# Kernel tuning notes

Hardware: AMD Instinct MI355X
Metric: run time of the kernel (lower is better)

## Reference

```python
import jax, jax.numpy as jnp
import numpy as np

INPUT_DIM = 1024
ATTN_DIM = 1024
B, S = 4, 4096


def setup_inputs() -> dict:
    key = jax.random.key(0)
    ks = jax.random.split(key, 9)
    def xavier(k, shape):
        fan_in, fan_out = shape[1], shape[0]
        limit = (6.0 / (fan_in + fan_out)) ** 0.5
        return jax.random.uniform(k, shape, jnp.float32, -limit, limit)
    return {
        "x": jax.random.normal(ks[0], (B, S, INPUT_DIM), jnp.float32),
        "Wq": xavier(ks[1], (ATTN_DIM, INPUT_DIM)),
        "bq": jnp.zeros((ATTN_DIM,), jnp.float32),
        "Wk": xavier(ks[2], (ATTN_DIM, INPUT_DIM)),
        "bk": jnp.zeros((ATTN_DIM,), jnp.float32),
        "Wv": xavier(ks[3], (ATTN_DIM, INPUT_DIM)),
        "bv": jnp.zeros((ATTN_DIM,), jnp.float32),
        "Wo": xavier(ks[4], (INPUT_DIM, ATTN_DIM)),
        "bo": jnp.zeros((INPUT_DIM,), jnp.float32),
    }


def reference(x, Wq, bq, Wk, bk, Wv, bv, Wo, bo):
    # Linear layers: y = x @ W^T + b (torch convention, W is [out, in])
    q = jnp.einsum("bsd,ad->bsa", x, Wq) + bq  # [B,S,A]
    k = jnp.einsum("bsd,ad->bsa", x, Wk) + bk
    v = jnp.einsum("bsd,ad->bsa", x, Wv) + bv
    scale = 1.0 / jnp.sqrt(jnp.float32(q.shape[-1]))
    scores = jnp.einsum("bqa,bka->bqk", q, k) * scale  # [B,S,S] full score matrix
    attn = jax.nn.softmax(scores, axis=-1)
    ctx = jnp.einsum("bqk,bka->bqa", attn, v)  # [B,S,A]
    return jnp.einsum("bsa,da->bsd", ctx, Wo) + bo
```

## Files before the change

kernel.cpp:

```cpp
#include <hip/hip_runtime.h>
#include <hip/hip_bf16.h>
#include <cstdint>

#define GLOBAL_AS __attribute__((address_space(1)))
#define LDS_AS    __attribute__((address_space(3)))

typedef __bf16 v8bf __attribute__((ext_vector_type(8)));
typedef __bf16 v4bf __attribute__((ext_vector_type(4)));
typedef float  v4f  __attribute__((ext_vector_type(4)));

struct P2 { __bf16* p[2]; };
struct P4 { __bf16* p[4]; };

template <int SWZ, int LBN, int LBM, int LNZ>
__device__ __forceinline__ void remap(int& bn, int& bm, int& bz) {
    if constexpr (!SWZ) {
        bn = blockIdx.x; bm = blockIdx.y; bz = blockIdx.z;
    } else {
        const unsigned f = blockIdx.x + (blockIdx.y << LBN) + (blockIdx.z << (LBN + LBM));
        const unsigned xcd = f & 7u, slot = f >> 3;
        constexpr unsigned T = (1u << (LNZ + LBM)) >> 3;
        const unsigned p = xcd * T + (slot >> LBN);
        bn = (int)(slot & ((1u << LBN) - 1u));
        bm = (int)(p & ((1u << LBM) - 1u));
        bz = (int)(p >> LBM);
    }
}

__device__ __forceinline__ void kloop(const __bf16* __restrict__ Abase, int lda,
                                      const __bf16* __restrict__ Bbase, int ldb,
                                      int K, __bf16* As, __bf16* Bs,
                                      v4f (&acc)[4][4], int wave, int lane)
{
    const int wr = wave >> 1, wc = wave & 1;
    const int quad = lane >> 4, l15 = lane & 15;
    const int ar = lane >> 2;
    const int ac = (lane & 3) * 8;

    for (int kt = 0; kt < K; kt += 32) {
        __syncthreads();
#pragma unroll
        for (int i = 0; i < 2; i++) {
            const int r = wave * 32 + i * 16;
            __builtin_amdgcn_global_load_lds(
                (const GLOBAL_AS void*)(Abase + (size_t)(r + ar) * lda + kt + ac),
                (LDS_AS void*)(As + r * 32), 16, 0, 0);
            __builtin_amdgcn_global_load_lds(
                (const GLOBAL_AS void*)(Bbase + (size_t)(r + ar) * ldb + kt + ac),
                (LDS_AS void*)(Bs + r * 32), 16, 0, 0);
        }
        __syncthreads();

        v8bf aF[4], bF[4];
#pragma unroll
        for (int i = 0; i < 4; i++)
            aF[i] = *(const v8bf*)(As + (wr * 64 + i * 16 + l15) * 32 + quad * 8);
#pragma unroll
        for (int j = 0; j < 4; j++)
            bF[j] = *(const v8bf*)(Bs + (wc * 64 + j * 16 + l15) * 32 + quad * 8);
#pragma unroll
        for (int i = 0; i < 4; i++)
#pragma unroll
            for (int j = 0; j < 4; j++)
                acc[i][j] = __builtin_amdgcn_mfma_f32_16x16x32_bf16(aF[i], bF[j], acc[i][j], 0, 0, 0);
    }
}

template <typename OutT, int SWZ, int LBN, int LBM, int LNZ>
__global__ void gemm_bt(const __bf16* __restrict__ A, int lda, long long sA,
                        const __bf16* __restrict__ B, int ldb, long long sB,
                        OutT* __restrict__ C, int ldc, long long sC,
                        int K,
                        const float* __restrict__ bias_col,
                        const float* __restrict__ bias_row)
{
    __shared__ __align__(16) __bf16 As[128 * 32];
    __shared__ __align__(16) __bf16 Bs[128 * 32];
    const int tid = threadIdx.x, wave = tid >> 6, lane = tid & 63;
    const int wr = wave >> 1, wc = wave & 1, quad = lane >> 4, l15 = lane & 15;
    int bn, bm, bz;
    remap<SWZ, LBN, LBM, LNZ>(bn, bm, bz);
    A += (long long)bz * sA;
    B += (long long)bz * sB;
    C += (long long)bz * sC;

    v4f acc[4][4];
#pragma unroll
    for (int i = 0; i < 4; i++)
#pragma unroll
        for (int j = 0; j < 4; j++) acc[i][j] = (v4f){0.f, 0.f, 0.f, 0.f};

    kloop(A + (size_t)(bm * 128) * lda, lda, B + (size_t)(bn * 128) * ldb, ldb,
          K, As, Bs, acc, wave, lane);

#pragma unroll
    for (int i = 0; i < 4; i++) {
        const int row0 = bm * 128 + wr * 64 + i * 16 + quad * 4;
#pragma unroll
        for (int j = 0; j < 4; j++) {
            const int col = bn * 128 + wc * 64 + j * 16 + l15;
            const float bc = bias_col ? bias_col[col] : 0.f;
#pragma unroll
            for (int r = 0; r < 4; r++) {
                float v = acc[i][j][r] + bc;
                if (bias_row) v += bias_row[row0 + r];
                C[(size_t)(row0 + r) * ldc + col] = (OutT)v;
            }
        }
    }
}

template <int SWZ, int LBN, int LBM, int LNZ>
__global__ void gemm_exp(const __bf16* __restrict__ A, int lda, long long sA,
                         const __bf16* __restrict__ B, int ldb, long long sB,
                         P2 Eout, int ldc,
                         float* __restrict__ rowsum, int rsStride, int K)
{
    __shared__ __align__(16) __bf16 As[128 * 32];
    __shared__ __align__(16) __bf16 Bs[128 * 32];
    const int tid = threadIdx.x, wave = tid >> 6, lane = tid & 63;
    const int wr = wave >> 1, wc = wave & 1, quad = lane >> 4, l15 = lane & 15;
    int bn, bm, bz;
    remap<SWZ, LBN, LBM, LNZ>(bn, bm, bz);
    A += (long long)bz * sA;
    B += (long long)bz * sB;
    __bf16* C = Eout.p[bz];
    float* rs = rowsum + (long long)bz * rsStride;

    v4f acc[4][4];
#pragma unroll
    for (int i = 0; i < 4; i++)
#pragma unroll
        for (int j = 0; j < 4; j++) acc[i][j] = (v4f){0.f, 0.f, 0.f, 0.f};

    kloop(A + (size_t)(bm * 128) * lda, lda, B + (size_t)(bn * 128) * ldb, ldb,
          K, As, Bs, acc, wave, lane);

#pragma unroll
    for (int i = 0; i < 4; i++) {
        const int row0 = bm * 128 + wr * 64 + i * 16 + quad * 4;
        float part[4] = {0.f, 0.f, 0.f, 0.f};
#pragma unroll
        for (int j = 0; j < 4; j++) {
            const int col = bn * 128 + wc * 64 + j * 16 + l15;
#pragma unroll
            for (int r = 0; r < 4; r++) {
                float e = __expf(acc[i][j][r]);
                C[(size_t)(row0 + r) * ldc + col] = (__bf16)e;
                part[r] += e;
            }
        }
#pragma unroll
        for (int r = 0; r < 4; r++) {
#pragma unroll
            for (int off = 1; off < 16; off <<= 1)
                part[r] += __shfl_xor(part[r], off, 16);
        }
        if (l15 == 0) {
#pragma unroll
            for (int r = 0; r < 4; r++) atomicAdd(&rs[row0 + r], part[r]);
        }
    }
}

template <int SWZ, int LBN, int LBM, int LNZ>
__global__ void gemm_av(P4 Ain, int lda,
                        const __bf16* __restrict__ Bv, int ldb, long long sB,
                        __bf16* __restrict__ C, int ldc, long long sC,
                        const float* __restrict__ rowsum, int rsStride, int K)
{
    __shared__ __align__(16) __bf16 As[128 * 32];
    __shared__ __align__(16) __bf16 Bs[128 * 32];
    const int tid = threadIdx.x, wave = tid >> 6, lane = tid & 63;
    const int wr = wave >> 1, wc = wave & 1, quad = lane >> 4, l15 = lane & 15;
    int bn, bm, bz;
    remap<SWZ, LBN, LBM, LNZ>(bn, bm, bz);
    const __bf16* A = Ain.p[bz];
    const __bf16* B = Bv + (long long)bz * sB;
    C += (long long)bz * sC;
    const float* rs = rowsum + (long long)bz * rsStride;

    v4f acc[4][4];
#pragma unroll
    for (int i = 0; i < 4; i++)
#pragma unroll
        for (int j = 0; j < 4; j++) acc[i][j] = (v4f){0.f, 0.f, 0.f, 0.f};

    kloop(A + (size_t)(bm * 128) * lda, lda, B + (size_t)(bn * 128) * ldb, ldb,
          K, As, Bs, acc, wave, lane);

#pragma unroll
    for (int i = 0; i < 4; i++) {
        const int row0 = bm * 128 + wr * 64 + i * 16 + quad * 4;
        float inv[4];
#pragma unroll
        for (int r = 0; r < 4; r++) inv[r] = 1.0f / rs[row0 + r];
#pragma unroll
        for (int j = 0; j < 4; j++) {
            const int col = bn * 128 + wc * 64 + j * 16 + l15;
#pragma unroll
            for (int r = 0; r < 4; r++)
                C[(size_t)(row0 + r) * ldc + col] = (__bf16)(acc[i][j][r] * inv[r]);
        }
    }
}

__global__ void cvt_f32_bf16(const float* __restrict__ in, __bf16* __restrict__ out, int n4) {
    int i = blockIdx.x * blockDim.x + threadIdx.x;
    if (i >= n4) return;
    float4 f = ((const float4*)in)[i];
    v4bf o;
    o[0] = (__bf16)f.x; o[1] = (__bf16)f.y; o[2] = (__bf16)f.z; o[3] = (__bf16)f.w;
    ((v4bf*)out)[i] = o;
}

__global__ void cvt_w4(const float* __restrict__ w0, const float* __restrict__ w1,
                       const float* __restrict__ w2, const float* __restrict__ w3,
                       __bf16* __restrict__ dst, int n4, float wscale0) {
    const float* s = blockIdx.y == 0 ? w0 : blockIdx.y == 1 ? w1 : blockIdx.y == 2 ? w2 : w3;
    const float sc = blockIdx.y == 0 ? wscale0 : 1.f;
    int i = blockIdx.x * blockDim.x + threadIdx.x;
    if (i >= n4) return;
    float4 f = ((const float4*)s)[i];
    v4bf o;
    o[0] = (__bf16)(f.x * sc); o[1] = (__bf16)(f.y * sc);
    o[2] = (__bf16)(f.z * sc); o[3] = (__bf16)(f.w * sc);
    ((v4bf*)(dst + (size_t)blockIdx.y * n4 * 4))[i] = o;
}

__global__ void concat_bias2(const float* __restrict__ b0, const float* __restrict__ b1,
                             float* __restrict__ dst, int n, float s0) {
    int i = blockIdx.x * blockDim.x + threadIdx.x;
    if (i < n) dst[i] = b0[i] * s0;
    else if (i < 2 * n) dst[i] = b1[i - n];
}

__global__ void zero_f32(float* __restrict__ p, int n) {
    int i = blockIdx.x * blockDim.x + threadIdx.x;
    if (i < n) p[i] = 0.f;
}

extern "C" void kernel_launch(void* const* d_in, const int* in_sizes, int n_in,
                              void* d_out, int out_size, void* d_ws, size_t ws_size,
                              hipStream_t stream)
{
    const float* x  = (const float*)d_in[0];
    const float* Wq = (const float*)d_in[1];
    const float* bq = (const float*)d_in[2];
    const float* Wk = (const float*)d_in[3];
    const float* bk = (const float*)d_in[4];
    const float* Wv = (const float*)d_in[5];
    const float* bv = (const float*)d_in[6];
    const float* Wo = (const float*)d_in[7];
    const float* bo = (const float*)d_in[8];
    float* out = (float*)d_out;

    constexpr int B = 4, S = 4096, D = 1024;
    constexpr long long MS = (long long)B * S;
    constexpr float scale = 0.03125f;

    char* w = (char*)d_ws;
    size_t used = 0;
    auto alloc = [&](size_t bytes) -> char* {
        char* p = w + used;
        used += (bytes + 255) & ~(size_t)255;
        return p;
    };
    __bf16* xb  = (__bf16*)alloc((size_t)MS * D * 2);
    __bf16* wqb = (__bf16*)alloc(4 * (size_t)D * D * 2);
    __bf16* wvb = wqb + 2 * (size_t)D * D;
    __bf16* wob = wqb + 3 * (size_t)D * D;
    float*  bqk = (float*)alloc(2 * D * 4);
    float*  rsm = (float*)alloc((size_t)B * S * 4);
    __bf16* qk  = (__bf16*)alloc((size_t)MS * 2 * D * 2);
    __bf16* vT  = (__bf16*)alloc((size_t)D * MS * 2);
    __bf16* Efr = (__bf16*)alloc(3 * (size_t)S * S * 2);
    __bf16* ctx = xb;
    if (used > ws_size) return;

    const long long SS = (long long)S * S;
    const long long qs = (long long)S * 2 * D;

    zero_f32<<<(B * S + 255) / 256, 256, 0, stream>>>(rsm, B * S);
    {
        int n4 = (int)(MS * D / 4);
        cvt_f32_bf16<<<(n4 + 255) / 256, 256, 0, stream>>>(x, xb, n4);
    }
    cvt_w4<<<dim3(D * D / 4 / 256, 4), 256, 0, stream>>>(Wq, Wk, Wv, Wo, wqb, D * D / 4, scale);
    concat_bias2<<<(2 * D + 255) / 256, 256, 0, stream>>>(bq, bk, bqk, D, scale);

    const dim3 blk(256);
    gemm_bt<__bf16, 1, 4, 7, 0><<<dim3(2 * D / 128, MS / 128), blk, 0, stream>>>(
        xb, D, 0, wqb, D, 0, qk, 2 * D, 0, D, bqk, nullptr);
    gemm_bt<__bf16, 0, 0, 0, 0><<<dim3(MS / 128, D / 128), blk, 0, stream>>>(
        wvb, D, 0, xb, D, 0, vT, (int)MS, 0, D, nullptr, bv);

    P2 e0; e0.p[0] = Efr;          e0.p[1] = Efr + SS;
    P2 e1; e1.p[0] = Efr + 2 * SS; e1.p[1] = qk;
    gemm_exp<1, 5, 5, 1><<<dim3(S / 128, S / 128, 2), blk, 0, stream>>>(
        qk, 2 * D, qs, qk + D, 2 * D, qs, e0, S, rsm, S, D);
    gemm_exp<1, 5, 5, 1><<<dim3(S / 128, S / 128, 2), blk, 0, stream>>>(
        qk + 2 * qs, 2 * D, qs, qk + D + 2 * qs, 2 * D, qs, e1, S, rsm + 2 * S, S, D);

    P4 ea; ea.p[0] = Efr; ea.p[1] = Efr + SS; ea.p[2] = Efr + 2 * SS; ea.p[3] = qk;
    gemm_av<1, 3, 5, 2><<<dim3(D / 128, S / 128, B), blk, 0, stream>>>(
        ea, S, vT, (int)MS, S, ctx, D, (long long)S * D, rsm, S, S);

    gemm_bt<float, 1, 3, 7, 0><<<dim3(D / 128, MS / 128), blk, 0, stream>>>(
        ctx, D, 0, wob, D, 0, out, D, 0, D, bo, nullptr);
}
```

Before: 641.8 us.

## Replace GEMM mainloop with 256x256 tile, 8-wave, multi-stage pipelined kloop

Swaps the simple 128x128, 4-wave, K=32 single-buffered GEMM loop for a 256x256 tile computed by 8 waves, using K=64 steps, two LDS stage sets split into half-tiles, XOR-swizzled LDS layout, and explicit waitcnt/barrier interleaving so global-to-LDS loads overlap MFMA work. It also raises MFMA priority with s_setprio. The aim is higher arithmetic intensity per LDS byte, fewer bank conflicts, and hidden load latency across all GEMMs. In exchange it uses 128KB of LDS per block, needs more accumulator registers, produces fewer blocks per GEMM, and requires K to be a multiple of 128.

```diff
diff --git a/kernel.cpp b/kernel.cpp
--- a/kernel.cpp
+++ b/kernel.cpp
@@ -11,6 +11,11 @@
 
 struct P2 { __bf16* p[2]; };
 struct P4 { __bf16* p[4]; };
+
+#define BAR()   __builtin_amdgcn_s_barrier()
+#define LGKM0() asm volatile("s_waitcnt lgkmcnt(0)" ::: "memory")
+#define LGKM8() asm volatile("s_waitcnt lgkmcnt(8)" ::: "memory")
+#define VMC6()  asm volatile("s_waitcnt vmcnt(6)" ::: "memory")
 
 template <int SWZ, int LBN, int LBM, int LNZ>
 __device__ __forceinline__ void remap(int& bn, int& bm, int& bz) {
@@ -27,81 +32,178 @@
     }
 }
 
-__device__ __forceinline__ void kloop(const __bf16* __restrict__ Abase, int lda,
-                                      const __bf16* __restrict__ Bbase, int ldb,
-                                      int K, __bf16* As, __bf16* Bs,
-                                      v4f (&acc)[4][4], int wave, int lane)
+template <int IB, int JB>
+__device__ __forceinline__ void mmq(v4f (&acc)[8][4], const v8bf (&As)[4][2],
+                                    const v8bf (&Bs)[2][2]) {
+    __builtin_amdgcn_s_setprio(1);
+#pragma unroll
+    for (int i = 0; i < 4; ++i)
+#pragma unroll
+        for (int j = 0; j < 2; ++j)
+#pragma unroll
+            for (int ks = 0; ks < 2; ++ks)
+                acc[IB + i][JB + j] = __builtin_amdgcn_mfma_f32_16x16x32_bf16(
+                    As[i][ks], Bs[j][ks], acc[IB + i][JB + j], 0, 0, 0);
+    __builtin_amdgcn_s_setprio(0);
+}
+
+__device__ __forceinline__ void kloop256(
+    const __bf16* __restrict__ A, int lda,
+    const __bf16* __restrict__ B, int ldb, int K,
+    __bf16* lds, v4f (&acc)[8][4], int tid)
 {
-    const int wr = wave >> 1, wc = wave & 1;
+    const int wave = tid >> 6, lane = tid & 63;
     const int quad = lane >> 4, l15 = lane & 15;
-    const int ar = lane >> 2;
-    const int ac = (lane & 3) * 8;
-
-    for (int kt = 0; kt < K; kt += 32) {
-        __syncthreads();
-#pragma unroll
-        for (int i = 0; i < 2; i++) {
-            const int r = wave * 32 + i * 16;
+    const int wm = wave >> 2, wn = wave & 3;
+
+    int ldsoff[2]; size_t offA[2], offB[2];
+#pragma unroll
+    for (int l = 0; l < 2; ++l) {
+        const int rr = (l * 512 + tid) >> 3;
+        const int ce = ((tid & 7) * 8) ^ ((rr & 4) ? 16 : 0);
+        offA[l] = (size_t)(((rr & ~63) << 1) + (rr & 63)) * lda + ce;
+        offB[l] = (size_t)(((rr & ~31) << 1) + (rr & 31)) * ldb + ce;
+        ldsoff[l] = (l * 512 + wave * 64) * 8;
+    }
+    const __bf16* Ah1 = A + (size_t)64 * lda;
+    const __bf16* Bh1 = B + (size_t)32 * ldb;
+
+    auto stA = [&](const __bf16* G, int kt, __bf16* region) {
+#pragma unroll
+        for (int l = 0; l < 2; ++l)
             __builtin_amdgcn_global_load_lds(
-                (const GLOBAL_AS void*)(Abase + (size_t)(r + ar) * lda + kt + ac),
-                (LDS_AS void*)(As + r * 32), 16, 0, 0);
+                (const GLOBAL_AS void*)(G + offA[l] + kt),
+                (LDS_AS void*)(region + ldsoff[l]), 16, 0, 0);
+    };
+    auto stB = [&](const __bf16* G, int kt, __bf16* region) {
+#pragma unroll
+        for (int l = 0; l < 2; ++l)
             __builtin_amdgcn_global_load_lds(
-                (const GLOBAL_AS void*)(Bbase + (size_t)(r + ar) * ldb + kt + ac),
-                (LDS_AS void*)(Bs + r * 32), 16, 0, 0);
-        }
-        __syncthreads();
-
-        v8bf aF[4], bF[4];
-#pragma unroll
-        for (int i = 0; i < 4; i++)
-            aF[i] = *(const v8bf*)(As + (wr * 64 + i * 16 + l15) * 32 + quad * 8);
-#pragma unroll
-        for (int j = 0; j < 4; j++)
-            bF[j] = *(const v8bf*)(Bs + (wc * 64 + j * 16 + l15) * 32 + quad * 8);
-#pragma unroll
-        for (int i = 0; i < 4; i++)
-#pragma unroll
-            for (int j = 0; j < 4; j++)
-                acc[i][j] = __builtin_amdgcn_mfma_f32_16x16x32_bf16(aF[i], bF[j], acc[i][j], 0, 0, 0);
+                (const GLOBAL_AS void*)(G + offB[l] + kt),
+                (LDS_AS void*)(region + ldsoff[l]), 16, 0, 0);
+    };
+
+    const int qsw = (quad << 4) ^ ((l15 & 4) ? 32 : 0);
+    const int laneA = ((wm * 64 + l15) << 7) + qsw;
+    const int laneB = ((wn * 32 + l15) << 7) + qsw;
+
+    v8bf Aset[4][2], Ba[2][2], Bb[2][2];
+    auto ldA = [&](const __bf16* region) {
+        const char* p = (const char*)region + laneA;
+#pragma unroll
+        for (int i = 0; i < 4; ++i)
+#pragma unroll
+            for (int ks = 0; ks < 2; ++ks)
+                Aset[i][ks] = *(const v8bf*)(p + i * 2048 + ks * 64);
+    };
+    auto ldB = [&](const __bf16* region, v8bf (&Bs)[2][2]) {
+        const char* p = (const char*)region + laneB;
+#pragma unroll
+        for (int j = 0; j < 2; ++j)
+#pragma unroll
+            for (int ks = 0; ks < 2; ++ks)
+                Bs[j][ks] = *(const v8bf*)(p + j * 2048 + ks * 64);
+    };
+
+    __bf16* const Ra0 = lds;
+    __bf16* const Ra1 = lds + 8192;
+    __bf16* const Rb0 = lds + 16384;
+    __bf16* const Rb1 = lds + 24576;
+    __bf16* const Sa0 = lds + 32768;
+    __bf16* const Sa1 = lds + 40960;
+    __bf16* const Sb0 = lds + 49152;
+    __bf16* const Sb1 = lds + 57344;
+
+    const int NT = K >> 6;
+    const int kcap = K - 64;
+
+    stA(A, 0, Ra0); stB(B, 0, Rb0); stB(Bh1, 0, Rb1); stA(Ah1, 0, Ra1);
+    stA(A, 64, Sa0); stB(B, 64, Sb0); stB(Bh1, 64, Sb1);
+    VMC6(); BAR();
+
+    for (int it = 0; it < (NT >> 1); ++it) {
+        const int u = it << 1;
+        int ktA = (u + 2) << 6; if (ktA > kcap) ktA = kcap;
+        int ktB = (u + 3) << 6; if (ktB > kcap) ktB = kcap;
+        const int kt1 = (u + 1) << 6;
+        ldA(Ra0); ldB(Rb0, Ba);
+        stA(Ah1, kt1, Sa1);
+        LGKM8(); BAR(); LGKM0();
+        mmq<0, 0>(acc, Aset, Ba);
+        BAR();
+        ldB(Rb1, Bb);
+        stA(A, ktA, Ra0);
+        BAR(); LGKM0();
+        mmq<0, 2>(acc, Aset, Bb);
+        BAR();
+        ldA(Ra1);
+        stB(B, ktA, Rb0);
+        BAR(); LGKM0();
+        mmq<4, 2>(acc, Aset, Bb);
+        BAR();
+        stB(Bh1, ktA, Rb1);
+        BAR(); LGKM0();
+        mmq<4, 0>(acc, Aset, Ba);
+        VMC6(); BAR();
+        ldA(Sa0); ldB(Sb0, Ba);
+        stA(Ah1, ktA, Ra1);
+        LGKM8(); BAR(); LGKM0();
+        mmq<0, 0>(acc, Aset, Ba);
+        BAR();
+        ldB(Sb1, Bb);
+        stA(A, ktB, Sa0);
+        BAR(); LGKM0();
+        mmq<0, 2>(acc, Aset, Bb);
+        BAR();
+        ldA(Sa1);
+        stB(B, ktB, Sb0);
+        BAR(); LGKM0();
+        mmq<4, 2>(acc, Aset, Bb);
+        BAR();
+        stB(Bh1, ktB, Sb1);
+        BAR(); LGKM0();
+        mmq<4, 0>(acc, Aset, Ba);
+        VMC6(); BAR();
     }
 }
 
 template <typename OutT, int SWZ, int LBN, int LBM, int LNZ>
-__global__ void gemm_bt(const __bf16* __restrict__ A, int lda, long long sA,
-                        const __bf16* __restrict__ B, int ldb, long long sB,
-                        OutT* __restrict__ C, int ldc, long long sC,
-                        int K,
-                        const float* __restrict__ bias_col,
-                        const float* __restrict__ bias_row)
+__global__ __launch_bounds__(512, 2)
+void gemm_bt(const __bf16* __restrict__ A, int lda, long long sA,
+             const __bf16* __restrict__ B, int ldb, long long sB,
+             OutT* __restrict__ C, int ldc, long long sC,
+             int K,
+             const float* __restrict__ bias_col,
+             const float* __restrict__ bias_row)
 {
-    __shared__ __align__(16) __bf16 As[128 * 32];
-    __shared__ __align__(16) __bf16 Bs[128 * 32];
+    __shared__ __align__(16) __bf16 lds[2 * 4 * 8192];
     const int tid = threadIdx.x, wave = tid >> 6, lane = tid & 63;
-    const int wr = wave >> 1, wc = wave & 1, quad = lane >> 4, l15 = lane & 15;
+    const int quad = lane >> 4, l15 = lane & 15;
+    const int wm = wave >> 2, wn = wave & 3;
     int bn, bm, bz;
     remap<SWZ, LBN, LBM, LNZ>(bn, bm, bz);
     A += (long long)bz * sA;
     B += (long long)bz * sB;
     C += (long long)bz * sC;
 
-    v4f acc[4][4];
-#pragma unroll
-    for (int i = 0; i < 4; i++)
-#pragma unroll
-        for (int j = 0; j < 4; j++) acc[i][j] = (v4f){0.f, 0.f, 0.f, 0.f};
-
-    kloop(A + (size_t)(bm * 128) * lda, lda, B + (size_t)(bn * 128) * ldb, ldb,
-          K, As, Bs, acc, wave, lane);
-
-#pragma unroll
-    for (int i = 0; i < 4; i++) {
-        const int row0 = bm * 128 + wr * 64 + i * 16 + quad * 4;
-#pragma unroll
-        for (int j = 0; j < 4; j++) {
-            const int col = bn * 128 + wc * 64 + j * 16 + l15;
+    v4f acc[8][4];
+#pragma unroll
+    for (int i = 0; i < 8; ++i)
+#pragma unroll
+        for (int j = 0; j < 4; ++j) acc[i][j] = (v4f){0.f, 0.f, 0.f, 0.f};
+
+    kloop256(A + (size_t)bm * 256 * lda, lda, B + (size_t)bn * 256 * ldb, ldb,
+             K, lds, acc, tid);
+
+#pragma unroll
+    for (int i = 0; i < 8; ++i) {
+        const int row0 = bm * 256 + wm * 128 + i * 16 + quad * 4;
+#pragma unroll
+        for (int j = 0; j < 4; ++j) {
+            const int col = bn * 256 + wn * 64 + j * 16 + l15;
             const float bc = bias_col ? bias_col[col] : 0.f;
 #pragma unroll
-            for (int r = 0; r < 4; r++) {
+            for (int r = 0; r < 4; ++r) {
                 float v = acc[i][j][r] + bc;
                 if (bias_row) v += bias_row[row0 + r];
                 C[(size_t)(row0 + r) * ldc + col] = (OutT)v;
@@ -111,15 +213,16 @@
 }
 
 template <int SWZ, int LBN, int LBM, int LNZ>
-__global__ void gemm_exp(const __bf16* __restrict__ A, int lda, long long sA,
-                         const __bf16* __restrict__ B, int ldb, long long sB,
-                         P2 Eout, int ldc,
-                         float* __restrict__ rowsum, int rsStride, int K)
+__global__ __launch_bounds__(512, 2)
+void gemm_exp(const __bf16* __restrict__ A, int lda, long long sA,
+              const __bf16* __restrict__ B, int ldb, long long sB,
+              P2 Eout, int ldc,
+              float* __restrict__ rowsum, int rsStride, int K)
 {
-    __shared__ __align__(16) __bf16 As[128 * 32];
-    __shared__ __align__(16) __bf16 Bs[128 * 32];
+    __shared__ __align__(16) __bf16 lds[2 * 4 * 8192];
     const int tid = threadIdx.x, wave = tid >> 6, lane = tid & 63;
-    const int wr = wave >> 1, wc = wave & 1, quad = lane >> 4, l15 = lane & 15;
+    const int quad = lane >> 4, l15 = lane & 15;
+    const int wm = wave >> 2, wn = wave & 3;
     int bn, bm, bz;
     remap<SWZ, LBN, LBM, LNZ>(bn, bm, bz);
     A += (long long)bz * sA;
@@ -127,52 +230,53 @@
     __bf16* C = Eout.p[bz];
     float* rs = rowsum + (long long)bz * rsStride;
 
-    v4f acc[4][4];
-#pragma unroll
-    for (int i = 0; i < 4; i++)
-#pragma unroll
-        for (int j = 0; j < 4; j++) acc[i][j] = (v4f){0.f, 0.f, 0.f, 0.f};
-
-    kloop(A + (size_t)(bm * 128) * lda, lda, B + (size_t)(bn * 128) * ldb, ldb,
-          K, As, Bs, acc, wave, lane);
-
-#pragma unroll
-    for (int i = 0; i < 4; i++) {
-        const int row0 = bm * 128 + wr * 64 + i * 16 + quad * 4;
+    v4f acc[8][4];
+#pragma unroll
+    for (int i = 0; i < 8; ++i)
+#pragma unroll
+        for (int j = 0; j < 4; ++j) acc[i][j] = (v4f){0.f, 0.f, 0.f, 0.f};
+
+    kloop256(A + (size_t)bm * 256 * lda, lda, B + (size_t)bn * 256 * ldb, ldb,
+             K, lds, acc, tid);
+
+#pragma unroll
+    for (int i = 0; i < 8; ++i) {
+        const int row0 = bm * 256 + wm * 128 + i * 16 + quad * 4;
         float part[4] = {0.f, 0.f, 0.f, 0.f};
 #pragma unroll
-        for (int j = 0; j < 4; j++) {
-            const int col = bn * 128 + wc * 64 + j * 16 + l15;
-#pragma unroll
-            for (int r = 0; r < 4; r++) {
+        for (int j = 0; j < 4; ++j) {
+            const int col = bn * 256 + wn * 64 + j * 16 + l15;
+#pragma unroll
+            for (int r = 0; r < 4; ++r) {
                 float e = __expf(acc[i][j][r]);
                 C[(size_t)(row0 + r) * ldc + col] = (__bf16)e;
                 part[r] += e;
             }
         }
 #pragma unroll
-        for (int r = 0; r < 4; r++) {
+        for (int r = 0; r < 4; ++r) {
 #pragma unroll
             for (int off = 1; off < 16; off <<= 1)
                 part[r] += __shfl_xor(part[r], off, 16);
         }
         if (l15 == 0) {
 #pragma unroll
-            for (int r = 0; r < 4; r++) atomicAdd(&rs[row0 + r], part[r]);
+            for (int r = 0; r < 4; ++r) atomicAdd(&rs[row0 + r], part[r]);
         }
     }
 }
 
 template <int SWZ, int LBN, int LBM, int LNZ>
-__global__ void gemm_av(P4 Ain, int lda,
-                        const __bf16* __restrict__ Bv, int ldb, long long sB,
-                        __bf16* __restrict__ C, int ldc, long long sC,
-                        const float* __restrict__ rowsum, int rsStride, int K)
+__global__ __launch_bounds__(512, 2)
+void gemm_av(P4 Ain, int lda,
+             const __bf16* __restrict__ Bv, int ldb, long long sB,
+             __bf16* __restrict__ C, int ldc, long long sC,
+             const float* __restrict__ rowsum, int rsStride, int K)
 {
-    __shared__ __align__(16) __bf16 As[128 * 32];
-    __shared__ __align__(16) __bf16 Bs[128 * 32];
+    __shared__ __align__(16) __bf16 lds[2 * 4 * 8192];
     const int tid = threadIdx.x, wave = tid >> 6, lane = tid & 63;
-    const int wr = wave >> 1, wc = wave & 1, quad = lane >> 4, l15 = lane & 15;
+    const int quad = lane >> 4, l15 = lane & 15;
+    const int wm = wave >> 2, wn = wave & 3;
     int bn, bm, bz;
     remap<SWZ, LBN, LBM, LNZ>(bn, bm, bz);
     const __bf16* A = Ain.p[bz];
@@ -180,26 +284,26 @@
     C += (long long)bz * sC;
     const float* rs = rowsum + (long long)bz * rsStride;
 
-    v4f acc[4][4];
-#pragma unroll
-    for (int i = 0; i < 4; i++)
-#pragma unroll
-        for (int j = 0; j < 4; j++) acc[i][j] = (v4f){0.f, 0.f, 0.f, 0.f};
-
-    kloop(A + (size_t)(bm * 128) * lda, lda, B + (size_t)(bn * 128) * ldb, ldb,
-          K, As, Bs, acc, wave, lane);
-
-#pragma unroll
-    for (int i = 0; i < 4; i++) {
-        const int row0 = bm * 128 + wr * 64 + i * 16 + quad * 4;
+    v4f acc[8][4];
+#pragma unroll
+    for (int i = 0; i < 8; ++i)
+#pragma unroll
+        for (int j = 0; j < 4; ++j) acc[i][j] = (v4f){0.f, 0.f, 0.f, 0.f};
+
+    kloop256(A + (size_t)bm * 256 * lda, lda, B + (size_t)bn * 256 * ldb, ldb,
+             K, lds, acc, tid);
+
+#pragma unroll
+    for (int i = 0; i < 8; ++i) {
+        const int row0 = bm * 256 + wm * 128 + i * 16 + quad * 4;
         float inv[4];
 #pragma unroll
-        for (int r = 0; r < 4; r++) inv[r] = 1.0f / rs[row0 + r];
-#pragma unroll
-        for (int j = 0; j < 4; j++) {
-            const int col = bn * 128 + wc * 64 + j * 16 + l15;
-#pragma unroll
-            for (int r = 0; r < 4; r++)
+        for (int r = 0; r < 4; ++r) inv[r] = 1.0f / rs[row0 + r];
+#pragma unroll
+        for (int j = 0; j < 4; ++j) {
+            const int col = bn * 256 + wn * 64 + j * 16 + l15;
+#pragma unroll
+            for (int r = 0; r < 4; ++r)
                 C[(size_t)(row0 + r) * ldc + col] = (__bf16)(acc[i][j][r] * inv[r]);
         }
     }
@@ -289,23 +393,23 @@
     cvt_w4<<<dim3(D * D / 4 / 256, 4), 256, 0, stream>>>(Wq, Wk, Wv, Wo, wqb, D * D / 4, scale);
     concat_bias2<<<(2 * D + 255) / 256, 256, 0, stream>>>(bq, bk, bqk, D, scale);
 
-    const dim3 blk(256);
-    gemm_bt<__bf16, 1, 4, 7, 0><<<dim3(2 * D / 128, MS / 128), blk, 0, stream>>>(
+    const dim3 blk(512);
+    gemm_bt<__bf16, 1, 3, 6, 0><<<dim3(2 * D / 256, MS / 256), blk, 0, stream>>>(
         xb, D, 0, wqb, D, 0, qk, 2 * D, 0, D, bqk, nullptr);
-    gemm_bt<__bf16, 0, 0, 0, 0><<<dim3(MS / 128, D / 128), blk, 0, stream>>>(
+    gemm_bt<__bf16, 0, 0, 0, 0><<<dim3(MS / 256, D / 256), blk, 0, stream>>>(
         wvb, D, 0, xb, D, 0, vT, (int)MS, 0, D, nullptr, bv);
 
     P2 e0; e0.p[0] = Efr;          e0.p[1] = Efr + SS;
     P2 e1; e1.p[0] = Efr + 2 * SS; e1.p[1] = qk;
-    gemm_exp<1, 5, 5, 1><<<dim3(S / 128, S / 128, 2), blk, 0, stream>>>(
+    gemm_exp<1, 4, 4, 1><<<dim3(S / 256, S / 256, 2), blk, 0, stream>>>(
         qk, 2 * D, qs, qk + D, 2 * D, qs, e0, S, rsm, S, D);
-    gemm_exp<1, 5, 5, 1><<<dim3(S / 128, S / 128, 2), blk, 0, stream>>>(
+    gemm_exp<1, 4, 4, 1><<<dim3(S / 256, S / 256, 2), blk, 0, stream>>>(
         qk + 2 * qs, 2 * D, qs, qk + D + 2 * qs, 2 * D, qs, e1, S, rsm + 2 * S, S, D);
 
     P4 ea; ea.p[0] = Efr; ea.p[1] = Efr + SS; ea.p[2] = Efr + 2 * SS; ea.p[3] = qk;
-    gemm_av<1, 3, 5, 2><<<dim3(D / 128, S / 128, B), blk, 0, stream>>>(
+    gemm_av<1, 2, 4, 2><<<dim3(D / 256, S / 256, B), blk, 0, stream>>>(
         ea, S, vT, (int)MS, S, ctx, D, (long long)S * D, rsm, S, S);
 
-    gemm_bt<float, 1, 3, 7, 0><<<dim3(D / 128, MS / 128), blk, 0, stream>>>(
+    gemm_bt<float, 1, 2, 6, 0><<<dim3(D / 256, MS / 256), blk, 0, stream>>>(
         ctx, D, 0, wob, D, 0, out, D, 0, D, bo, nullptr);
 }
```

Measured after the change: 599.5 us. 6.6% less time.
